# Optimization experiments

Hardware: AMD Instinct MI355X
Metric: run time of the kernel (lower is better)

Reference implementation:

```python
import jax, jax.numpy as jnp
import numpy as np

B, S_DEC, S_ENC, D, H = 2, 2048, 2048, 1024, 16
HD = D // H  # 64


def setup_inputs() -> dict:
    key = jax.random.key(0)
    ks = jax.random.split(key, 12)
    s = 0.02
    return {
        "dec_hidden_state": jax.random.normal(ks[0], (B, S_DEC, D), jnp.float32),
        "enc_hidden_state": jax.random.normal(ks[1], (B, S_ENC, D), jnp.float32),
        "mask": jnp.ones((B, S_ENC, S_DEC), jnp.int32),
        "Wq": jax.random.normal(ks[2], (H, D, HD), jnp.float32) * s,
        "bq": jax.random.normal(ks[3], (H, HD), jnp.float32) * s,
        "Wk": jax.random.normal(ks[4], (H, D, HD), jnp.float32) * s,
        "bk": jax.random.normal(ks[5], (H, HD), jnp.float32) * s,
        "Wv": jax.random.normal(ks[6], (H, D, HD), jnp.float32) * s,
        "bv": jax.random.normal(ks[7], (H, HD), jnp.float32) * s,
        "Wo": jax.random.normal(ks[8], (D, D), jnp.float32) * s,
        "bo": jax.random.normal(ks[9], (D,), jnp.float32) * s,
    }


def reference(dec_hidden_state, enc_hidden_state, mask, Wq, bq, Wk, bk, Wv, bv, Wo, bo):
    # NOTE: original module swaps args: query <- enc_hidden_state, key/value <- dec_hidden_state.
    # q: [B,H,S_enc,HD], k/v: [B,H,S_dec,HD]
    q = jnp.einsum("bqd,hdk->bhqk", enc_hidden_state, Wq) + bq[None, :, None, :]
    k = jnp.einsum("bsd,hdk->bhsk", dec_hidden_state, Wk) + bk[None, :, None, :]
    v = jnp.einsum("bsd,hdk->bhsk", dec_hidden_state, Wv) + bv[None, :, None, :]
    scores = jnp.einsum("bhqk,bhsk->bhqs", q, k) / jnp.sqrt(jnp.asarray(HD, q.dtype))
    scores = jnp.where(mask[:, None, :, :] == 0, jnp.asarray(-jnp.inf, scores.dtype), scores)
    weights = jax.nn.softmax(scores, axis=-1)
    attn = jnp.einsum("bhqs,bhsk->bhqk", weights, v)  # [B,H,S_enc,HD]
    # concat heads along last dim (same order as torch.cat over head list)
    attn = jnp.transpose(attn, (0, 2, 1, 3)).reshape(B, S_ENC, D)
    return attn @ Wo + bo
```

## Files before the change

kernel.cpp:

```cpp
#include <hip/hip_runtime.h>
#include <math.h>
#include <stdint.h>


typedef unsigned short ushort_t;
typedef __attribute__((ext_vector_type(8))) short short8;
typedef __attribute__((ext_vector_type(4))) short short4v;
typedef __attribute__((ext_vector_type(4))) float floatx4;

__device__ __forceinline__ ushort_t f2bf(float x){
  unsigned u = __float_as_uint(x);
  u += 0x7fffu + ((u >> 16) & 1u);
  return (ushort_t)(u >> 16);
}
__device__ __forceinline__ unsigned pk2bf(float a, float b){
#if __has_builtin(__builtin_amdgcn_cvt_pk_bf16_f32)
  typedef __attribute__((ext_vector_type(2))) __bf16 bf2_t;
  bf2_t r = __builtin_amdgcn_cvt_pk_bf16_f32(a, b);
  return *(unsigned*)&r;
#else
  return (unsigned)f2bf(a) | ((unsigned)f2bf(b) << 16);
#endif
}
__device__ __forceinline__ floatx4 mfma16(short8 a, short8 b, floatx4 c){
  return __builtin_amdgcn_mfma_f32_16x16x32_bf16(a, b, c, 0, 0, 0);
}
#if __has_builtin(__builtin_amdgcn_mfma_f32_16x16x16bf16_1k)
__device__ __forceinline__ floatx4 mfma_pv(short4v a, short4v b, floatx4 c){
  return __builtin_amdgcn_mfma_f32_16x16x16bf16_1k(a, b, c, 0, 0, 0);
}
#else
__device__ __forceinline__ floatx4 mfma_pv(short4v a, short4v b, floatx4 c){
  short8 a8 = {a[0], a[1], a[2], a[3], 0, 0, 0, 0};
  short8 b8 = {b[0], b[1], b[2], b[3], 0, 0, 0, 0};
  return mfma16(a8, b8, c);
}
#endif
__device__ __forceinline__ void async_copy16(const void* g, void* l){
  __builtin_amdgcn_global_load_lds((const __attribute__((address_space(1))) void*)g,
                                   (__attribute__((address_space(3))) void*)l,
                                   16, 0, 0);
}

__global__ __launch_bounds__(256)
void prep_kernel(const float* __restrict__ enc, const float* __restrict__ dec,
                 const float* __restrict__ Wq, const float* __restrict__ Wk,
                 const float* __restrict__ Wv, const float* __restrict__ Wo,
                 const int* __restrict__ mask,
                 ushort_t* __restrict__ encb, ushort_t* __restrict__ decb,
                 ushort_t* __restrict__ WqT, ushort_t* __restrict__ WkT,
                 ushort_t* __restrict__ WvT, ushort_t* __restrict__ WoT,
                 unsigned long long* __restrict__ mb)
{
  __shared__ float t[64][65];
  const int bx = blockIdx.x, tid = threadIdx.x;
  if (bx < 8192){
    const float* src = (bx < 4096) ? enc : dec;
    ushort_t*    dst = (bx < 4096) ? encb : decb;
    int i = ((bx & 4095) * 256 + tid) * 4;
    const float4 v = *(const float4*)(src + i);
    unsigned long long p = (unsigned long long)f2bf(v.x)
                         | ((unsigned long long)f2bf(v.y) << 16)
                         | ((unsigned long long)f2bf(v.z) << 32)
                         | ((unsigned long long)f2bf(v.w) << 48);
    *(unsigned long long*)(dst + i) = p;
  } else if (bx < 8960){
    const int id = bx - 8192;
    const int zz = id >> 4, yy = id & 15;
    const int which = zz >> 4, head = zz & 15;
    const float* src = (which == 0) ? Wq : (which == 1) ? Wk : Wv;
    ushort_t*    dst = (which == 0) ? WqT : (which == 1) ? WkT : WvT;
    const long sb = (long)head * 65536;
    const int r0 = yy * 64;
    #pragma unroll
    for (int i = 0; i < 16; i++){
      int idx = i*256 + tid;
      int r = idx >> 6, c = idx & 63;
      t[r][c] = src[sb + (long)(r0 + r)*64 + c];
    }
    __syncthreads();
    #pragma unroll
    for (int i = 0; i < 16; i++){
      int idx = i*256 + tid;
      int cr = idx >> 6, rc = idx & 63;
      dst[sb + (long)cr*1024 + r0 + rc] = f2bf(t[rc][cr]);
    }
  } else if (bx < 9216){
    const int id = bx - 8960;
    const int r0 = (id >> 4) * 64, c0 = (id & 15) * 64;
    #pragma unroll
    for (int i = 0; i < 16; i++){
      int idx = i*256 + tid;
      int r = idx >> 6, c = idx & 63;
      t[r][c] = Wo[(long)(r0 + r)*1024 + c0 + c];
    }
    __syncthreads();
    #pragma unroll
    for (int i = 0; i < 16; i++){
      int idx = i*256 + tid;
      int cr = idx >> 6, rc = idx & 63;
      WoT[(long)(c0 + cr)*1024 + r0 + rc] = f2bf(t[rc][cr]);
    }
  } else {
    long gid = (long)(bx - 9216) * 256 + tid;
    unsigned long long bal = __ballot(mask[gid] != 0);
    if ((tid & 63) == 0) mb[gid >> 6] = bal;
  }
}

__global__ __launch_bounds__(256, 3)
void gemm_qkv_kernel(const ushort_t* __restrict__ encb, const ushort_t* __restrict__ decb,
                     const ushort_t* __restrict__ WqT, const ushort_t* __restrict__ WkT,
                     const ushort_t* __restrict__ WvT,
                     const float* __restrict__ bq, const float* __restrict__ bk,
                     const float* __restrict__ bv,
                     ushort_t* __restrict__ Qb, ushort_t* __restrict__ Kbf,
                     ushort_t* __restrict__ Vtb)
{
  __shared__ ushort_t At[2*4096];
  __shared__ ushort_t Bt[2*4096];
  const int tid = threadIdx.x;
  const int wave = tid >> 6, lane = tid & 63;
  const int quad = lane >> 4, l16 = lane & 15;
  const int z = blockIdx.z;
  const ushort_t *A, *BT; const float* bias; ushort_t* outp;
  int m0, n0; long outAdj = 0;
  if (z == 0){ A = encb; BT = WqT; bias = bq; outp = Qb;  m0 = blockIdx.y*128; n0 = blockIdx.x*128; }
  else if (z == 1){ A = decb; BT = WkT; bias = bk; outp = Kbf; m0 = blockIdx.y*128; n0 = blockIdx.x*128; }
  else {
    int id = blockIdx.y*8 + blockIdx.x;
    int vb = id >> 7, rem = id & 127;
    m0 = ((rem >> 4) & 7) * 128; n0 = (rem & 15) * 128;
    A = WvT; BT = decb + (long)vb*2097152; bias = bv; outp = Vtb; outAdj = (long)vb*2097152;
  }
  const int K = 1024;

  const int c0 = tid, c1 = 256 + tid;
  const ushort_t* gA0 = A  + (long)(m0 + (c0 >> 2))*K + (c0 & 3)*8;
  const ushort_t* gA1 = A  + (long)(m0 + (c1 >> 2))*K + (c1 & 3)*8;
  const ushort_t* gB0 = BT + (long)(n0 + (c0 >> 2))*K + (c0 & 3)*8;
  const ushort_t* gB1 = BT + (long)(n0 + (c1 >> 2))*K + (c1 & 3)*8;

  floatx4 acc[4][4];
  #pragma unroll
  for (int mt = 0; mt < 4; mt++)
    #pragma unroll
    for (int nt = 0; nt < 4; nt++)
      acc[mt][nt] = (floatx4){0.f, 0.f, 0.f, 0.f};

  async_copy16(gA0, &At[wave*512]);
  async_copy16(gA1, &At[(4+wave)*512]);
  async_copy16(gB0, &Bt[wave*512]);
  async_copy16(gB1, &Bt[(4+wave)*512]);
  gA0 += 32; gA1 += 32; gB0 += 32; gB1 += 32;

  const int moff = (wave & 1) * 64, noff = (wave >> 1) * 64;
  int cur = 0;
  for (int k0 = 0; k0 < K; k0 += 32){
    __syncthreads();
    if (k0 + 32 < K){
      const int nx = cur ^ 1;
      async_copy16(gA0, &At[nx*4096 + wave*512]);
      async_copy16(gA1, &At[nx*4096 + (4+wave)*512]);
      async_copy16(gB0, &Bt[nx*4096 + wave*512]);
      async_copy16(gB1, &Bt[nx*4096 + (4+wave)*512]);
      gA0 += 32; gA1 += 32; gB0 += 32; gB1 += 32;
    }
    short8 af[4], bfr[4];
    #pragma unroll
    for (int t = 0; t < 4; t++){
      af[t]  = *(const short8*)&At[cur*4096 + (moff + t*16 + l16)*32 + quad*8];
      bfr[t] = *(const short8*)&Bt[cur*4096 + (noff + t*16 + l16)*32 + quad*8];
    }
    #pragma unroll
    for (int mt = 0; mt < 4; mt++)
      #pragma unroll
      for (int nt = 0; nt < 4; nt++)
        acc[mt][nt] = mfma16(af[mt], bfr[nt], acc[mt][nt]);
    cur ^= 1;
  }

  #pragma unroll
  for (int mt = 0; mt < 4; mt++){
    #pragma unroll
    for (int nt = 0; nt < 4; nt++){
      const int col = n0 + noff + nt*16 + l16;
      const int rowb = m0 + moff + mt*16 + quad*4;
      #pragma unroll
      for (int reg = 0; reg < 4; reg++){
        const int row = rowb + reg;
        float v = acc[mt][nt][reg];
        if (z < 2){
          v += bias[col];
          long o = ((long)(row >> 11)*16 + (col >> 6))*131072
                 + (long)(row & 2047)*64 + (col & 63);
          outp[o] = f2bf(v);
        } else {
          v += bias[row];
          outp[outAdj + (long)row*2048 + col] = f2bf(v);
        }
      }
    }
  }
}

__global__ __launch_bounds__(256, 2)
void gemm_o_kernel(const ushort_t* __restrict__ A, const ushort_t* __restrict__ BT,
                   const float* __restrict__ bias, float* __restrict__ outf)
{
  __shared__ ushort_t At[2*4096];
  __shared__ ushort_t Bt[2*2048];
  const int tid = threadIdx.x;
  const int wave = tid >> 6, lane = tid & 63;
  const int quad = lane >> 4, l16 = lane & 15;
  const int m0 = blockIdx.y * 128, n0 = blockIdx.x * 64;
  const int K = 1024;

  const int c0 = tid, c1 = 256 + tid;
  const ushort_t* gA0 = A  + (long)(m0 + (c0 >> 2))*K + (c0 & 3)*8;
  const ushort_t* gA1 = A  + (long)(m0 + (c1 >> 2))*K + (c1 & 3)*8;
  const ushort_t* gB0 = BT + (long)(n0 + (c0 >> 2))*K + (c0 & 3)*8;

  floatx4 acc[4][2];
  #pragma unroll
  for (int mt = 0; mt < 4; mt++)
    #pragma unroll
    for (int nt = 0; nt < 2; nt++)
      acc[mt][nt] = (floatx4){0.f, 0.f, 0.f, 0.f};

  async_copy16(gA0, &At[wave*512]);
  async_copy16(gA1, &At[(4+wave)*512]);
  async_copy16(gB0, &Bt[wave*512]);
  gA0 += 32; gA1 += 32; gB0 += 32;

  const int moff = (wave & 1) * 64, noff = (wave >> 1) * 32;
  int cur = 0;
  for (int k0 = 0; k0 < K; k0 += 32){
    __syncthreads();
    if (k0 + 32 < K){
      const int nx = cur ^ 1;
      async_copy16(gA0, &At[nx*4096 + wave*512]);
      async_copy16(gA1, &At[nx*4096 + (4+wave)*512]);
      async_copy16(gB0, &Bt[nx*2048 + wave*512]);
      gA0 += 32; gA1 += 32; gB0 += 32;
    }
    short8 af[4], bfr[2];
    #pragma unroll
    for (int t = 0; t < 4; t++)
      af[t]  = *(const short8*)&At[cur*4096 + (moff + t*16 + l16)*32 + quad*8];
    #pragma unroll
    for (int t = 0; t < 2; t++)
      bfr[t] = *(const short8*)&Bt[cur*2048 + (noff + t*16 + l16)*32 + quad*8];
    #pragma unroll
    for (int mt = 0; mt < 4; mt++)
      #pragma unroll
      for (int nt = 0; nt < 2; nt++)
        acc[mt][nt] = mfma16(af[mt], bfr[nt], acc[mt][nt]);
    cur ^= 1;
  }

  #pragma unroll
  for (int mt = 0; mt < 4; mt++){
    #pragma unroll
    for (int nt = 0; nt < 2; nt++){
      const int col = n0 + noff + nt*16 + l16;
      const int rowb = m0 + moff + mt*16 + quad*4;
      #pragma unroll
      for (int reg = 0; reg < 4; reg++)
        outf[(long)(rowb + reg)*1024 + col] = acc[mt][nt][reg] + bias[col];
    }
  }
}

__global__ __launch_bounds__(512, 4)
void flash_attn_kernel(const ushort_t* __restrict__ Q, const ushort_t* __restrict__ Kb,
                       const ushort_t* __restrict__ Vt, const unsigned* __restrict__ mb,
                       ushort_t* __restrict__ aout)
{
  __shared__ ushort_t Kbuf[2*4608];
  __shared__ ushort_t Vbuf[2*4608];
  const int tid = threadIdx.x, wave = tid >> 6, lane = tid & 63;
  const int quad = lane >> 4, l16 = lane & 15;
  const int bh = blockIdx.x, qt = blockIdx.y;
  const int b = bh >> 4, h = bh & 15;
  const float C = 0.18033688011112042f;

  const ushort_t* KB = Kb + (long)bh*131072;
  const ushort_t* VB = Vt + (long)bh*131072;
  const int q0 = qt*128 + wave*16;

  short8 qf0 = *(const short8*)&Q[((long)bh*2048 + q0 + l16)*64 +      quad*8];
  short8 qf1 = *(const short8*)&Q[((long)bh*2048 + q0 + l16)*64 + 32 + quad*8];

  floatx4 accO[4];
  #pragma unroll
  for (int ht = 0; ht < 4; ht++) accO[ht] = (floatx4){0.f,0.f,0.f,0.f};
  float lsum = 0.f;

  const int srow = tid >> 3, scol = (tid & 7) * 8;
  const ushort_t* gKp = KB + srow*64 + scol;
  const ushort_t* gVp = VB + (long)srow*2048 + scol;
  const int loff = srow*72 + scol;

  const uint2* mb2 = (const uint2*)mb;
  const long mbase = (long)b*2048 + q0;

  short8 gk = *(const short8*)gKp;  gKp += 4096;
  short8 gv = *(const short8*)gVp;  gVp += 64;

  int cur = 0;
  for (int st = 0; st < 32; st++){
    *(short8*)&Kbuf[cur*4608 + loff] = gk;
    *(short8*)&Vbuf[cur*4608 + loff] = gv;
    __syncthreads();
    if (st < 31){
      gk = *(const short8*)gKp;  gKp += 4096;
      gv = *(const short8*)gVp;  gVp += 64;
    }
    const ushort_t* Kp = &Kbuf[cur*4608];
    const ushort_t* Vp = &Vbuf[cur*4608];

    uint2 mw = mb2[(mbase + l16)*32 + st];
    const bool uni = __all((mw.x & mw.y) == 0xFFFFFFFFu);

    #pragma unroll
    for (int mtile = 0; mtile < 4; mtile++){
      short8 kf0 = *(const short8*)&Kp[(mtile*16 + l16)*72 +      quad*8];
      short8 kf1 = *(const short8*)&Kp[(mtile*16 + l16)*72 + 32 + quad*8];
      floatx4 zz = (floatx4){0.f,0.f,0.f,0.f};
      zz = mfma16(kf0, qf0, zz);
      zz = mfma16(kf1, qf1, zz);
      float p0 = __builtin_amdgcn_exp2f(zz[0]*C);
      float p1 = __builtin_amdgcn_exp2f(zz[1]*C);
      float p2 = __builtin_amdgcn_exp2f(zz[2]*C);
      float p3 = __builtin_amdgcn_exp2f(zz[3]*C);
      if (__builtin_expect(!uni, 0)){
        const unsigned w = (mtile & 2) ? mw.y : mw.x;
        const int sh = (mtile & 1)*16 + quad*4;
        p0 = ((w >> (sh+0)) & 1u) ? p0 : 0.f;
        p1 = ((w >> (sh+1)) & 1u) ? p1 : 0.f;
        p2 = ((w >> (sh+2)) & 1u) ? p2 : 0.f;
        p3 = ((w >> (sh+3)) & 1u) ? p3 : 0.f;
      }
      lsum += (p0 + p1) + (p2 + p3);
      uint2 pk; pk.x = pk2bf(p0, p1); pk.y = pk2bf(p2, p3);
      const short4v pb = *(const short4v*)&pk;
      #pragma unroll
      for (int ht = 0; ht < 4; ht++){
        short4v vf = *(const short4v*)&Vp[(ht*16 + l16)*72 + mtile*16 + quad*4];
        accO[ht] = mfma_pv(vf, pb, accO[ht]);
      }
    }
    cur ^= 1;
  }

  lsum += __shfl_xor(lsum, 16);
  lsum += __shfl_xor(lsum, 32);
  const float inv = 1.0f / lsum;

  const long rowo = ((long)b*2048 + q0 + l16)*1024 + h*64;
  #pragma unroll
  for (int ht = 0; ht < 4; ht++){
    uint2 pk;
    pk.x = pk2bf(accO[ht][0]*inv, accO[ht][1]*inv);
    pk.y = pk2bf(accO[ht][2]*inv, accO[ht][3]*inv);
    *(unsigned long long*)&aout[rowo + ht*16 + quad*4] = *(unsigned long long*)&pk;
  }
}

extern "C" void kernel_launch(void* const* d_in, const int* in_sizes, int n_in,
                              void* d_out, int out_size, void* d_ws, size_t ws_size,
                              hipStream_t stream) {
  const float* dec  = (const float*)d_in[0];
  const float* enc  = (const float*)d_in[1];
  const int*   mask = (const int*)d_in[2];
  const float* Wq   = (const float*)d_in[3];
  const float* bq   = (const float*)d_in[4];
  const float* Wk   = (const float*)d_in[5];
  const float* bk   = (const float*)d_in[6];
  const float* Wv   = (const float*)d_in[7];
  const float* bv   = (const float*)d_in[8];
  const float* Wo   = (const float*)d_in[9];
  const float* bo   = (const float*)d_in[10];
  float* out = (float*)d_out;

  ushort_t* ws   = (ushort_t*)d_ws;
  ushort_t* encb = ws;
  ushort_t* decb = encb + 4194304;
  ushort_t* Qb   = decb + 4194304;
  ushort_t* Kbf  = Qb   + 4194304;
  ushort_t* Vtb  = Kbf  + 4194304;
  ushort_t* WqT  = Vtb  + 4194304;
  ushort_t* WkT  = WqT  + 1048576;
  ushort_t* WvT  = WkT  + 1048576;
  ushort_t* WoT  = WvT  + 1048576;
  unsigned* Mb   = (unsigned*)(WoT + 1048576);

  prep_kernel<<<41984, 256, 0, stream>>>(enc, dec, Wq, Wk, Wv, Wo, mask,
                                         encb, decb, WqT, WkT, WvT, WoT,
                                         (unsigned long long*)Mb);
  gemm_qkv_kernel<<<dim3(8,32,3), 256, 0, stream>>>(encb, decb, WqT, WkT, WvT,
                                                    bq, bk, bv, Qb, Kbf, Vtb);
  flash_attn_kernel<<<dim3(32,16,1), 512, 0, stream>>>(Qb, Kbf, Vtb, Mb, encb);
  gemm_o_kernel<<<dim3(16,32,1), 256, 0, stream>>>(encb, WoT, bo, out);
}
```

Measured before the change: 261.7 us.

## Swap MFMA operands for vectorized epilogue stores and shrink attention blocks

After: 258.3 us. No clear change (-1.3%).

```diff
diff --git a/kernel.cpp b/kernel.cpp
--- a/kernel.cpp
+++ b/kernel.cpp
@@ -176,7 +176,7 @@
     for (int mt = 0; mt < 4; mt++)
       #pragma unroll
       for (int nt = 0; nt < 4; nt++)
-        acc[mt][nt] = mfma16(af[mt], bfr[nt], acc[mt][nt]);
+        acc[mt][nt] = mfma16(bfr[nt], af[mt], acc[mt][nt]);
     cur ^= 1;
   }
 
@@ -184,21 +184,23 @@
   for (int mt = 0; mt < 4; mt++){
     #pragma unroll
     for (int nt = 0; nt < 4; nt++){
-      const int col = n0 + noff + nt*16 + l16;
-      const int rowb = m0 + moff + mt*16 + quad*4;
-      #pragma unroll
-      for (int reg = 0; reg < 4; reg++){
-        const int row = rowb + reg;
-        float v = acc[mt][nt][reg];
-        if (z < 2){
-          v += bias[col];
-          long o = ((long)(row >> 11)*16 + (col >> 6))*131072
-                 + (long)(row & 2047)*64 + (col & 63);
-          outp[o] = f2bf(v);
-        } else {
-          v += bias[row];
-          outp[outAdj + (long)row*2048 + col] = f2bf(v);
-        }
+      floatx4 v = acc[mt][nt];
+      if (z < 2){
+        const int s   = m0 + moff + mt*16 + l16;
+        const int ch0 = n0 + noff + nt*16 + quad*4;
+        const float4 b4 = *(const float4*)&bias[ch0];
+        uint2 pk;
+        pk.x = pk2bf(v[0] + b4.x, v[1] + b4.y);
+        pk.y = pk2bf(v[2] + b4.z, v[3] + b4.w);
+        *(unsigned long long*)&outp[(long)s*1024 + ch0] = *(unsigned long long*)&pk;
+      } else {
+        const int ch = m0 + moff + mt*16 + l16;
+        const int s0 = n0 + noff + nt*16 + quad*4;
+        const float bb = bias[ch];
+        uint2 pk;
+        pk.x = pk2bf(v[0] + bb, v[1] + bb);
+        pk.y = pk2bf(v[2] + bb, v[3] + bb);
+        *(unsigned long long*)&outp[outAdj + (long)ch*2048 + s0] = *(unsigned long long*)&pk;
       }
     }
   }
@@ -255,7 +257,7 @@
     for (int mt = 0; mt < 4; mt++)
       #pragma unroll
       for (int nt = 0; nt < 2; nt++)
-        acc[mt][nt] = mfma16(af[mt], bfr[nt], acc[mt][nt]);
+        acc[mt][nt] = mfma16(bfr[nt], af[mt], acc[mt][nt]);
     cur ^= 1;
   }
 
@@ -263,17 +265,21 @@
   for (int mt = 0; mt < 4; mt++){
     #pragma unroll
     for (int nt = 0; nt < 2; nt++){
-      const int col = n0 + noff + nt*16 + l16;
-      const int rowb = m0 + moff + mt*16 + quad*4;
-      #pragma unroll
-      for (int reg = 0; reg < 4; reg++)
-        outf[(long)(rowb + reg)*1024 + col] = acc[mt][nt][reg] + bias[col];
-    }
-  }
-}
-
-__global__ __launch_bounds__(512, 4)
-void flash_attn_kernel(const ushort_t* __restrict__ Q, const ushort_t* __restrict__ Kb,
+      const int s   = m0 + moff + mt*16 + l16;
+      const int ch0 = n0 + noff + nt*16 + quad*4;
+      const float4 b4 = *(const float4*)&bias[ch0];
+      float4 o;
+      o.x = acc[mt][nt][0] + b4.x;
+      o.y = acc[mt][nt][1] + b4.y;
+      o.z = acc[mt][nt][2] + b4.z;
+      o.w = acc[mt][nt][3] + b4.w;
+      *(float4*)&outf[(long)s*1024 + ch0] = o;
+    }
+  }
+}
+
+__global__ __launch_bounds__(256, 4)
+void flash_attn_kernel(const ushort_t* __restrict__ Qp, const ushort_t* __restrict__ Kp,
                        const ushort_t* __restrict__ Vt, const unsigned* __restrict__ mb,
                        ushort_t* __restrict__ aout)
 {
@@ -285,39 +291,48 @@
   const int b = bh >> 4, h = bh & 15;
   const float C = 0.18033688011112042f;
 
-  const ushort_t* KB = Kb + (long)bh*131072;
   const ushort_t* VB = Vt + (long)bh*131072;
-  const int q0 = qt*128 + wave*16;
-
-  short8 qf0 = *(const short8*)&Q[((long)bh*2048 + q0 + l16)*64 +      quad*8];
-  short8 qf1 = *(const short8*)&Q[((long)bh*2048 + q0 + l16)*64 + 32 + quad*8];
+  const int q0 = qt*64 + wave*16;
+
+  const long qrow = ((long)b*2048 + q0 + l16)*1024 + h*64;
+  short8 qf0 = *(const short8*)&Qp[qrow +      quad*8];
+  short8 qf1 = *(const short8*)&Qp[qrow + 32 + quad*8];
 
   floatx4 accO[4];
   #pragma unroll
   for (int ht = 0; ht < 4; ht++) accO[ht] = (floatx4){0.f,0.f,0.f,0.f};
   float lsum = 0.f;
 
-  const int srow = tid >> 3, scol = (tid & 7) * 8;
-  const ushort_t* gKp = KB + srow*64 + scol;
-  const ushort_t* gVp = VB + (long)srow*2048 + scol;
-  const int loff = srow*72 + scol;
+  const int c0 = tid, c1 = 256 + tid;
+  const ushort_t* gK0 = Kp + ((long)b*2048 + (c0 >> 3))*1024 + h*64 + (c0 & 7)*8;
+  const ushort_t* gK1 = Kp + ((long)b*2048 + (c1 >> 3))*1024 + h*64 + (c1 & 7)*8;
+  const ushort_t* gV0 = VB + (long)(c0 >> 3)*2048 + (c0 & 7)*8;
+  const ushort_t* gV1 = VB + (long)(c1 >> 3)*2048 + (c1 & 7)*8;
+  const int lo0 = (c0 >> 3)*72 + (c0 & 7)*8;
+  const int lo1 = (c1 >> 3)*72 + (c1 & 7)*8;
 
   const uint2* mb2 = (const uint2*)mb;
   const long mbase = (long)b*2048 + q0;
 
-  short8 gk = *(const short8*)gKp;  gKp += 4096;
-  short8 gv = *(const short8*)gVp;  gVp += 64;
+  short8 gk0 = *(const short8*)gK0;  gK0 += 65536;
+  short8 gk1 = *(const short8*)gK1;  gK1 += 65536;
+  short8 gv0 = *(const short8*)gV0;  gV0 += 64;
+  short8 gv1 = *(const short8*)gV1;  gV1 += 64;
 
   int cur = 0;
   for (int st = 0; st < 32; st++){
-    *(short8*)&Kbuf[cur*4608 + loff] = gk;
-    *(short8*)&Vbuf[cur*4608 + loff] = gv;
+    *(short8*)&Kbuf[cur*4608 + lo0] = gk0;
+    *(short8*)&Kbuf[cur*4608 + lo1] = gk1;
+    *(short8*)&Vbuf[cur*4608 + lo0] = gv0;
+    *(short8*)&Vbuf[cur*4608 + lo1] = gv1;
     __syncthreads();
     if (st < 31){
-      gk = *(const short8*)gKp;  gKp += 4096;
-      gv = *(const short8*)gVp;  gVp += 64;
-    }
-    const ushort_t* Kp = &Kbuf[cur*4608];
+      gk0 = *(const short8*)gK0;  gK0 += 65536;
+      gk1 = *(const short8*)gK1;  gK1 += 65536;
+      gv0 = *(const short8*)gV0;  gV0 += 64;
+      gv1 = *(const short8*)gV1;  gV1 += 64;
+    }
+    const ushort_t* Kt = &Kbuf[cur*4608];
     const ushort_t* Vp = &Vbuf[cur*4608];
 
     uint2 mw = mb2[(mbase + l16)*32 + st];
@@ -325,8 +340,8 @@
 
     #pragma unroll
     for (int mtile = 0; mtile < 4; mtile++){
-      short8 kf0 = *(const short8*)&Kp[(mtile*16 + l16)*72 +      quad*8];
-      short8 kf1 = *(const short8*)&Kp[(mtile*16 + l16)*72 + 32 + quad*8];
+      short8 kf0 = *(const short8*)&Kt[(mtile*16 + l16)*72 +      quad*8];
+      short8 kf1 = *(const short8*)&Kt[(mtile*16 + l16)*72 + 32 + quad*8];
       floatx4 zz = (floatx4){0.f,0.f,0.f,0.f};
       zz = mfma16(kf0, qf0, zz);
       zz = mfma16(kf1, qf1, zz);
@@ -401,6 +416,6 @@
                                          (unsigned long long*)Mb);
   gemm_qkv_kernel<<<dim3(8,32,3), 256, 0, stream>>>(encb, decb, WqT, WkT, WvT,
                                                     bq, bk, bv, Qb, Kbf, Vtb);
-  flash_attn_kernel<<<dim3(32,16,1), 512, 0, stream>>>(Qb, Kbf, Vtb, Mb, encb);
+  flash_attn_kernel<<<dim3(32,32,1), 256, 0, stream>>>(Qb, Kbf, Vtb, Mb, encb);
   gemm_o_kernel<<<dim3(16,32,1), 256, 0, stream>>>(encb, WoT, bo, out);
 }
```
